# Kernel tuning notes

Hardware: AMD Instinct MI355X
Metric: run time of the kernel (lower is better)

## Reference

```python
import jax, jax.numpy as jnp
import numpy as np

EPS = 1e-7

def squash(s, axis=-1):
    # s * ||s||^2 / (1 + ||s||^2) / ||s||
    sq_norm = jnp.sum(jnp.square(s), axis=axis, keepdims=True)
    scale = sq_norm / (1.0 + sq_norm) / jnp.sqrt(sq_norm + EPS)
    return scale * s

def setup_inputs() -> dict:
    key = jax.random.key(0)
    k1, k2 = jax.random.split(key)
    B, I, K = 64, 2048, 16   # batch, input_num_capsule, input_dim_capsule
    N, D = 32, 32            # num_capsule, dim_capsule
    inputs = jax.random.normal(k1, (B, I, K), dtype=jnp.float32)
    W = jax.random.normal(k2, (N, I, D, K), dtype=jnp.float32) * 0.05
    return {"inputs": inputs, "W": W}

def reference(inputs, W, routings=3):
    # u_hat[b,n,i,d] = sum_k inputs[b,i,k] * W[n,i,d,k]
    # (tile over n + per-sample batch_dot in the original, fused here)
    u_hat = jnp.einsum('bik,nidk->bnid', inputs, W)  # [B,N,I,D]
    B, N, I, D = u_hat.shape
    b = jnp.zeros((B, N, I), dtype=u_hat.dtype)
    outputs = None
    for r in range(routings):
        c = jax.nn.softmax(b, axis=1)                          # softmax over num_capsule
        s = jnp.einsum('bni,bnid->bnd', c, u_hat)              # weighted sum over input caps
        outputs = squash(s)                                    # [B,N,D]
        if r < routings - 1:
            b = b + jnp.einsum('bnd,bnid->bni', outputs, u_hat)  # agreement update
    return outputs
```

## Files before the change

### kernel.cpp

```cpp
#include <hip/hip_runtime.h>
#include <hip/hip_bf16.h>
#include <math.h>

#define B_ 64
#define I_ 2048
#define K_ 16
#define N_ 32
#define D_ 32
#define SCH_ 16

typedef __attribute__((ext_vector_type(8))) short short8_t;
typedef __attribute__((ext_vector_type(4))) float f32x4_t;

#define OFF_INT   0u
#define OFF_CT    2097152u
#define OFF_BT    6291456u
#define OFF_SPART 10485760u
#define OFF_OFRAG 11534336u
#define OFF_XFRAG 11599872u
#define OFF_WFS   12648448u
#define OFF_WFU   29425664u

__device__ __forceinline__ unsigned int pk_bf16(float lo, float hi) {
    union { __hip_bfloat162 h2; unsigned int u; } cv;
    cv.h2 = __float22bfloat162_rn(float2{lo, hi});
    return cv.u;
}

__global__ __launch_bounds__(256) void k_prep(const float* __restrict__ in,
                                              float* __restrict__ inT,
                                              uint4* __restrict__ xfrag) {
    __shared__ float lds[B_][K_ + 1];
    const int i = blockIdx.x;
    const int t = threadIdx.x;
    const int b = t >> 2, kq = t & 3;
    const float4 v = *(const float4*)(in + ((size_t)b * I_ + i) * K_ + kq * 4);
    lds[b][kq * 4 + 0] = v.x; lds[b][kq * 4 + 1] = v.y;
    lds[b][kq * 4 + 2] = v.z; lds[b][kq * 4 + 3] = v.w;
    __syncthreads();
#pragma unroll
    for (int q = 0; q < 4; ++q) {
        const int j = t + q * 256;
        const int k = j >> 6, bb = j & 63;
        inT[(size_t)i * (K_ * B_) + j] = lds[bb][k];
    }
    if (t < 128) {
        const int m = t >> 5, r = t & 31, gl = r >> 4, kl = r & 15;
        const int bb = m * 16 + kl, k0 = 8 * gl;
        union { unsigned int u[4]; uint4 q; } o;
#pragma unroll
        for (int p = 0; p < 4; ++p)
            o.u[p] = pk_bf16(lds[bb][k0 + 2 * p], lds[bb][k0 + 2 * p + 1]);
        xfrag[((size_t)m * 1024 + (i >> 1)) * 64 + (2 * (i & 1) + gl) * 16 + kl] = o.q;
    }
}

__global__ __launch_bounds__(256) void k_wpack(const float* __restrict__ W,
                                               uint4* __restrict__ wfs,
                                               uint4* __restrict__ wfu) {
    __shared__ __align__(16) float lds[2048];
    const int c = blockIdx.x;
    const int n = blockIdx.y;
    const int t = threadIdx.x;
    const float4* s4 = (const float4*)(W + ((size_t)n * I_ + c * 4) * 512);
    float4* d4 = (float4*)lds;
    d4[t] = s4[t];
    d4[t + 256] = s4[t + 256];
    __syncthreads();
    {
        const int il = t >> 6, l = t & 63, g = l >> 4, kl = l & 15;
        const float* base = lds + il * 512;
        union { unsigned int u[4]; uint4 q; } o;
#pragma unroll
        for (int p = 0; p < 4; ++p)
            o.u[p] = pk_bf16(base[(8 * g + 2 * p) * 16 + kl],
                             base[(8 * g + 2 * p + 1) * 16 + kl]);
        wfu[((size_t)n * I_ + c * 4 + il) * 64 + l] = o.q;
    }
    {
        const int kkl = t >> 7, r = t & 127, nt = r >> 6, l = r & 63, g = l >> 4;
        const float* p = lds + kkl * 1024 + (g >> 1) * 512 + nt * 256
                         + (l & 15) * 16 + (g & 1) * 8;
        const float4 f0 = *(const float4*)p;
        const float4 f1 = *(const float4*)(p + 4);
        union { unsigned int u[4]; uint4 q; } o;
        o.u[0] = pk_bf16(f0.x, f0.y); o.u[1] = pk_bf16(f0.z, f0.w);
        o.u[2] = pk_bf16(f1.x, f1.y); o.u[3] = pk_bf16(f1.z, f1.w);
        wfs[(((size_t)n * 1024 + c * 2 + kkl) * 2 + nt) * 64 + l] = o.q;
    }
}

template<int UNIFORM>
__global__ __launch_bounds__(512, 2) void k_sweep_mfma(const uint4* __restrict__ wfs,
                                                       const uint4* __restrict__ xfrag,
                                                       const float* __restrict__ cT,
                                                       float* __restrict__ spart) {
    __shared__ float red[2][B_][D_ + 1];
    const int n = blockIdx.y, ch = blockIdx.x;
    const int t = threadIdx.x, w = t >> 6, l = t & 63;
    const int m = w >> 1, ks = w & 1;

    f32x4_t acc0 = {0.f, 0.f, 0.f, 0.f};
    f32x4_t acc1 = {0.f, 0.f, 0.f, 0.f};

    const uint4* xf = xfrag + (size_t)m * 65536 + l;
    const uint4* wf = wfs + (size_t)n * (1024 * 128) + l;
    const int kk0 = ch * 64 + ks * 32;

    for (int tt = 0; tt < 32; ++tt) {
        const int kk = kk0 + tt;
        union { uint4 q; unsigned int u[4]; } xv;
        xv.q = xf[(size_t)kk * 64];
        union { unsigned int u[4]; short8_t v; } af;
        if (UNIFORM) {
            af.u[0] = xv.u[0]; af.u[1] = xv.u[1];
            af.u[2] = xv.u[2]; af.u[3] = xv.u[3];
        } else {
            const float c = cT[((size_t)n * I_ + 2 * kk + (l >> 5)) * B_
                               + m * 16 + (l & 15)];
#pragma unroll
            for (int p = 0; p < 4; ++p) {
                const unsigned int uu = xv.u[p];
                const float lo = __uint_as_float(uu << 16);
                const float hi = __uint_as_float(uu & 0xffff0000u);
                af.u[p] = pk_bf16(lo * c, hi * c);
            }
        }
        union { uint4 q; short8_t v; } b0, b1;
        b0.q = wf[(size_t)kk * 128];
        b1.q = wf[(size_t)kk * 128 + 64];

        acc0 = __builtin_amdgcn_mfma_f32_16x16x32_bf16(af.v, b0.v, acc0, 0, 0, 0);
        acc1 = __builtin_amdgcn_mfma_f32_16x16x32_bf16(af.v, b1.v, acc1, 0, 0, 0);
    }

#pragma unroll
    for (int r = 0; r < 4; ++r) {
        const int row = m * 16 + (l >> 4) * 4 + r;
        red[ks][row][(l & 15)]      = acc0[r];
        red[ks][row][16 + (l & 15)] = acc1[r];
    }
    __syncthreads();
#pragma unroll
    for (int q = 0; q < 4; ++q) {
        const int j = q * 512 + t;
        const int b = j >> 5, d = j & 31;
        spart[((size_t)n * SCH_ + ch) * (B_ * D_) + j] = red[0][b][d] + red[1][b][d];
    }
}

template<int FINAL>
__global__ __launch_bounds__(256) void k_reduce(const float* __restrict__ spart,
                                                unsigned int* __restrict__ ofrag_u32,
                                                float* __restrict__ out,
                                                float prescale) {
    const int gt = blockIdx.x * 256 + threadIdx.x;
    const int n = gt >> 11;
    const int rem = gt & 2047;
    const int b = rem >> 5, d = rem & 31;
    const float* sp = spart + (size_t)n * (SCH_ * B_ * D_) + rem;
    float s = 0.f;
#pragma unroll
    for (int p = 0; p < SCH_; ++p) s += sp[p * (B_ * D_)];
    s *= prescale;

    float sq = s * s;
#pragma unroll
    for (int off = 16; off >= 1; off >>= 1) sq += __shfl_xor(sq, off, 64);
    const float scale = sq / ((1.0f + sq) * sqrtf(sq + 1e-7f));
    const float o = scale * s;
    if (FINAL) {
        out[((size_t)b * N_ + n) * D_ + d] = o;
    } else {
        const float o_next = __shfl_down(o, 1, 64);
        if ((d & 1) == 0) {
            const unsigned int val = pk_bf16(o, o_next);
            const int l = (d >> 3) * 16 + (b & 15);
            ofrag_u32[(((n * 4 + (b >> 4)) * 64) + l) * 4 + ((d & 7) >> 1)] = val;
        }
    }
}

template<int FIRST>
__global__ __launch_bounds__(512, 2) void k_updsm(const uint4* __restrict__ wfu,
                                                  const float* __restrict__ inT,
                                                  const uint4* __restrict__ ofrag,
                                                  float* __restrict__ bT,
                                                  float* __restrict__ cT) {
    const int t = threadIdx.x, w = t >> 6, l = t & 63;
    const int btile = w & 3;
    const int i = blockIdx.x * 2 + (w >> 2);
    const int g = l >> 4, kl = l & 15;
    const int bp = btile * 16 + kl;

    float x4[4];
    {
        const float* xp = inT + (size_t)i * (K_ * B_) + bp;
#pragma unroll
        for (int r = 0; r < 4; ++r) x4[r] = xp[(4 * g + r) * B_];
    }

    float bn[N_];
#pragma unroll
    for (int n = 0; n < N_; ++n) {
        union { uint4 q; short8_t v; } of, af;
        of.q = ofrag[(n * 4 + btile) * 64 + l];
        af.q = wfu[((size_t)n * I_ + i) * 64 + l];
        f32x4_t acc = {0.f, 0.f, 0.f, 0.f};
        acc = __builtin_amdgcn_mfma_f32_16x16x32_bf16(af.v, of.v, acc, 0, 0, 0);
        float gp = 0.f;
#pragma unroll
        for (int r = 0; r < 4; ++r) gp = fmaf(acc[r], x4[r], gp);
        gp += __shfl_xor(gp, 16, 64);
        gp += __shfl_xor(gp, 32, 64);
        const size_t bi = ((size_t)n * I_ + i) * B_ + bp;
        if (FIRST) {
            if (l < 16) bT[bi] = gp;
        } else {
            gp += bT[bi];
        }
        bn[n] = gp;
    }

    float mx = bn[0];
#pragma unroll
    for (int n = 1; n < N_; ++n) mx = fmaxf(mx, bn[n]);
    float sum = 0.f;
#pragma unroll
    for (int n = 0; n < N_; ++n) { bn[n] = __expf(bn[n] - mx); sum += bn[n]; }
    const float inv = 1.0f / sum;
    if (l < 16) {
#pragma unroll
        for (int n = 0; n < N_; ++n)
            cT[((size_t)n * I_ + i) * B_ + bp] = bn[n] * inv;
    }
}

extern "C" void kernel_launch(void* const* d_in, const int* in_sizes, int n_in,
                              void* d_out, int out_size, void* d_ws, size_t ws_size,
                              hipStream_t stream) {
    const float* inputs = (const float*)d_in[0];
    const float* W      = (const float*)d_in[1];
    float* out = (float*)d_out;
    float* ws  = (float*)d_ws;
    float* inT   = ws + OFF_INT;
    float* cT    = ws + OFF_CT;
    float* bT    = ws + OFF_BT;
    float* spart = ws + OFF_SPART;
    unsigned int* ofrag_u32 = (unsigned int*)(ws + OFF_OFRAG);
    uint4* ofrag = (uint4*)(ws + OFF_OFRAG);
    uint4* xfrag = (uint4*)(ws + OFF_XFRAG);
    uint4* wfs   = (uint4*)(ws + OFF_WFS);
    uint4* wfu   = (uint4*)(ws + OFF_WFU);

    k_prep<<<I_, 256, 0, stream>>>(inputs, inT, xfrag);
    k_wpack<<<dim3(512, N_), 256, 0, stream>>>(W, wfs, wfu);
    k_sweep_mfma<1><<<dim3(SCH_, N_), 512, 0, stream>>>(wfs, xfrag, cT, spart);
    k_reduce<0><<<256, 256, 0, stream>>>(spart, ofrag_u32, out, 1.0f / N_);
    k_updsm<1><<<I_ / 2, 512, 0, stream>>>(wfu, inT, ofrag, bT, cT);
    k_sweep_mfma<0><<<dim3(SCH_, N_), 512, 0, stream>>>(wfs, xfrag, cT, spart);
    k_reduce<0><<<256, 256, 0, stream>>>(spart, ofrag_u32, out, 1.0f);
    k_updsm<0><<<I_ / 2, 512, 0, stream>>>(wfu, inT, ofrag, bT, cT);
    k_sweep_mfma<0><<<dim3(SCH_, N_), 512, 0, stream>>>(wfs, xfrag, cT, spart);
    k_reduce<1><<<256, 256, 0, stream>>>(spart, ofrag_u32, out, 1.0f);
}
```

Before: 175.6 us.

## Use single plain bf16 copy of W for both sweep and agreement kernels

Replaces the two fragment-packed bf16 copies of W (wfs and wfu) with one straight bf16 conversion of W in its original layout, produced by a simple streaming kernel. Both the sweep and update kernels now index this shared buffer directly. The update kernel is restructured so each wave handles two input capsules: it computes x·W via MFMA with zero-masked halves, then dots the result with fp32 outputs read from a plain oT buffer, replacing the packed ofrag and the fp32 transposed inputs. The goal is to halve the weight packing writes and the workspace footprint, at the cost of doubled MFMA count and less fragment-friendly, more strided loads in the update kernel.

```diff
diff --git a/kernel.cpp b/kernel.cpp
--- a/kernel.cpp
+++ b/kernel.cpp
@@ -12,14 +12,12 @@
 typedef __attribute__((ext_vector_type(8))) short short8_t;
 typedef __attribute__((ext_vector_type(4))) float f32x4_t;
 
-#define OFF_INT   0u
-#define OFF_CT    2097152u
-#define OFF_BT    6291456u
-#define OFF_SPART 10485760u
-#define OFF_OFRAG 11534336u
-#define OFF_XFRAG 11599872u
-#define OFF_WFS   12648448u
-#define OFF_WFU   29425664u
+#define OFF_CT    0u
+#define OFF_BT    4194304u
+#define OFF_SPART 8388608u
+#define OFF_OT    9437184u
+#define OFF_XFRAG 9502720u
+#define OFF_WBF   10551296u
 
 __device__ __forceinline__ unsigned int pk_bf16(float lo, float hi) {
     union { __hip_bfloat162 h2; unsigned int u; } cv;
@@ -27,8 +25,19 @@
     return cv.u;
 }
 
+__global__ __launch_bounds__(256) void k_wconv(const float* __restrict__ W,
+                                               uint4* __restrict__ wbf4) {
+    const size_t tid = (size_t)blockIdx.x * 256 + threadIdx.x;
+    const float4* W4 = (const float4*)W;
+    const float4 a = W4[2 * tid];
+    const float4 b = W4[2 * tid + 1];
+    uint4 o;
+    o.x = pk_bf16(a.x, a.y); o.y = pk_bf16(a.z, a.w);
+    o.z = pk_bf16(b.x, b.y); o.w = pk_bf16(b.z, b.w);
+    wbf4[tid] = o;
+}
+
 __global__ __launch_bounds__(256) void k_prep(const float* __restrict__ in,
-                                              float* __restrict__ inT,
                                               uint4* __restrict__ xfrag) {
     __shared__ float lds[B_][K_ + 1];
     const int i = blockIdx.x;
@@ -38,12 +47,6 @@
     lds[b][kq * 4 + 0] = v.x; lds[b][kq * 4 + 1] = v.y;
     lds[b][kq * 4 + 2] = v.z; lds[b][kq * 4 + 3] = v.w;
     __syncthreads();
-#pragma unroll
-    for (int q = 0; q < 4; ++q) {
-        const int j = t + q * 256;
-        const int k = j >> 6, bb = j & 63;
-        inT[(size_t)i * (K_ * B_) + j] = lds[bb][k];
-    }
     if (t < 128) {
         const int m = t >> 5, r = t & 31, gl = r >> 4, kl = r & 15;
         const int bb = m * 16 + kl, k0 = 8 * gl;
@@ -55,43 +58,8 @@
     }
 }
 
-__global__ __launch_bounds__(256) void k_wpack(const float* __restrict__ W,
-                                               uint4* __restrict__ wfs,
-                                               uint4* __restrict__ wfu) {
-    __shared__ __align__(16) float lds[2048];
-    const int c = blockIdx.x;
-    const int n = blockIdx.y;
-    const int t = threadIdx.x;
-    const float4* s4 = (const float4*)(W + ((size_t)n * I_ + c * 4) * 512);
-    float4* d4 = (float4*)lds;
-    d4[t] = s4[t];
-    d4[t + 256] = s4[t + 256];
-    __syncthreads();
-    {
-        const int il = t >> 6, l = t & 63, g = l >> 4, kl = l & 15;
-        const float* base = lds + il * 512;
-        union { unsigned int u[4]; uint4 q; } o;
-#pragma unroll
-        for (int p = 0; p < 4; ++p)
-            o.u[p] = pk_bf16(base[(8 * g + 2 * p) * 16 + kl],
-                             base[(8 * g + 2 * p + 1) * 16 + kl]);
-        wfu[((size_t)n * I_ + c * 4 + il) * 64 + l] = o.q;
-    }
-    {
-        const int kkl = t >> 7, r = t & 127, nt = r >> 6, l = r & 63, g = l >> 4;
-        const float* p = lds + kkl * 1024 + (g >> 1) * 512 + nt * 256
-                         + (l & 15) * 16 + (g & 1) * 8;
-        const float4 f0 = *(const float4*)p;
-        const float4 f1 = *(const float4*)(p + 4);
-        union { unsigned int u[4]; uint4 q; } o;
-        o.u[0] = pk_bf16(f0.x, f0.y); o.u[1] = pk_bf16(f0.z, f0.w);
-        o.u[2] = pk_bf16(f1.x, f1.y); o.u[3] = pk_bf16(f1.z, f1.w);
-        wfs[(((size_t)n * 1024 + c * 2 + kkl) * 2 + nt) * 64 + l] = o.q;
-    }
-}
-
 template<int UNIFORM>
-__global__ __launch_bounds__(512, 2) void k_sweep_mfma(const uint4* __restrict__ wfs,
+__global__ __launch_bounds__(512, 2) void k_sweep_mfma(const uint4* __restrict__ wbf4,
                                                        const uint4* __restrict__ xfrag,
                                                        const float* __restrict__ cT,
                                                        float* __restrict__ spart) {
@@ -99,12 +67,14 @@
     const int n = blockIdx.y, ch = blockIdx.x;
     const int t = threadIdx.x, w = t >> 6, l = t & 63;
     const int m = w >> 1, ks = w & 1;
+    const int g = l >> 4;
 
     f32x4_t acc0 = {0.f, 0.f, 0.f, 0.f};
     f32x4_t acc1 = {0.f, 0.f, 0.f, 0.f};
 
     const uint4* xf = xfrag + (size_t)m * 65536 + l;
-    const uint4* wf = wfs + (size_t)n * (1024 * 128) + l;
+    const uint4* wb = wbf4 + (size_t)n * (I_ * 64)
+                    + (size_t)(g >> 1) * 64 + (l & 15) * 2 + (g & 1);
     const int kk0 = ch * 64 + ks * 32;
 
     for (int tt = 0; tt < 32; ++tt) {
@@ -127,8 +97,8 @@
             }
         }
         union { uint4 q; short8_t v; } b0, b1;
-        b0.q = wf[(size_t)kk * 128];
-        b1.q = wf[(size_t)kk * 128 + 64];
+        b0.q = wb[(size_t)kk * 128];
+        b1.q = wb[(size_t)kk * 128 + 32];
 
         acc0 = __builtin_amdgcn_mfma_f32_16x16x32_bf16(af.v, b0.v, acc0, 0, 0, 0);
         acc1 = __builtin_amdgcn_mfma_f32_16x16x32_bf16(af.v, b1.v, acc1, 0, 0, 0);
@@ -151,7 +121,7 @@
 
 template<int FINAL>
 __global__ __launch_bounds__(256) void k_reduce(const float* __restrict__ spart,
-                                                unsigned int* __restrict__ ofrag_u32,
+                                                float* __restrict__ oT,
                                                 float* __restrict__ out,
                                                 float prescale) {
     const int gt = blockIdx.x * 256 + threadIdx.x;
@@ -172,67 +142,79 @@
     if (FINAL) {
         out[((size_t)b * N_ + n) * D_ + d] = o;
     } else {
-        const float o_next = __shfl_down(o, 1, 64);
-        if ((d & 1) == 0) {
-            const unsigned int val = pk_bf16(o, o_next);
-            const int l = (d >> 3) * 16 + (b & 15);
-            ofrag_u32[(((n * 4 + (b >> 4)) * 64) + l) * 4 + ((d & 7) >> 1)] = val;
-        }
+        oT[gt] = o;
     }
 }
 
 template<int FIRST>
-__global__ __launch_bounds__(512, 2) void k_updsm(const uint4* __restrict__ wfu,
-                                                  const float* __restrict__ inT,
-                                                  const uint4* __restrict__ ofrag,
+__global__ __launch_bounds__(512, 2) void k_updsm(const uint4* __restrict__ wbf4,
+                                                  const uint4* __restrict__ xfrag,
+                                                  const float* __restrict__ oT,
                                                   float* __restrict__ bT,
                                                   float* __restrict__ cT) {
     const int t = threadIdx.x, w = t >> 6, l = t & 63;
     const int btile = w & 3;
-    const int i = blockIdx.x * 2 + (w >> 2);
+    const int p = blockIdx.x * 2 + (w >> 2);
+    const int i_e = 2 * p;
     const int g = l >> 4, kl = l & 15;
     const int bp = btile * 16 + kl;
 
-    float x4[4];
-    {
-        const float* xp = inT + (size_t)i * (K_ * B_) + bp;
-#pragma unroll
-        for (int r = 0; r < 4; ++r) x4[r] = xp[(4 * g + r) * B_];
-    }
-
-    float bn[N_];
+    union { uint4 q; short8_t v; } xf;
+    xf.q = xfrag[((size_t)btile * 1024 + p) * 64 + l];
+
+    const int i_l = i_e + (g >> 1);
+    const uint4* wrow = wbf4 + (size_t)i_l * 64 + kl * 2 + (g & 1);
+    const uint4 z4 = {0u, 0u, 0u, 0u};
+
+    float bne[N_], bno[N_];
 #pragma unroll
     for (int n = 0; n < N_; ++n) {
-        union { uint4 q; short8_t v; } of, af;
-        of.q = ofrag[(n * 4 + btile) * 64 + l];
-        af.q = wfu[((size_t)n * I_ + i) * 64 + l];
-        f32x4_t acc = {0.f, 0.f, 0.f, 0.f};
-        acc = __builtin_amdgcn_mfma_f32_16x16x32_bf16(af.v, of.v, acc, 0, 0, 0);
-        float gp = 0.f;
-#pragma unroll
-        for (int r = 0; r < 4; ++r) gp = fmaf(acc[r], x4[r], gp);
-        gp += __shfl_xor(gp, 16, 64);
-        gp += __shfl_xor(gp, 32, 64);
-        const size_t bi = ((size_t)n * I_ + i) * B_ + bp;
+        const uint4* wb = wrow + (size_t)n * (I_ * 64);
+        const float* op = oT + (size_t)n * 2048 + bp * 32 + 4 * g;
+        float ge = 0.f, go = 0.f;
+#pragma unroll
+        for (int h = 0; h < 2; ++h) {
+            union { uint4 q; short8_t v; } av, ae, ao;
+            av.q = wb[32 * h];
+            ae.q = (g < 2) ? av.q : z4;
+            ao.q = (g < 2) ? z4 : av.q;
+            f32x4_t ce = {0.f, 0.f, 0.f, 0.f};
+            f32x4_t co = {0.f, 0.f, 0.f, 0.f};
+            ce = __builtin_amdgcn_mfma_f32_16x16x32_bf16(ae.v, xf.v, ce, 0, 0, 0);
+            co = __builtin_amdgcn_mfma_f32_16x16x32_bf16(ao.v, xf.v, co, 0, 0, 0);
+            const float4 o4 = *(const float4*)(op + 16 * h);
+            ge += ce[0] * o4.x + ce[1] * o4.y + ce[2] * o4.z + ce[3] * o4.w;
+            go += co[0] * o4.x + co[1] * o4.y + co[2] * o4.z + co[3] * o4.w;
+        }
+        ge += __shfl_xor(ge, 16, 64);  ge += __shfl_xor(ge, 32, 64);
+        go += __shfl_xor(go, 16, 64);  go += __shfl_xor(go, 32, 64);
+        const size_t be = ((size_t)n * I_ + i_e) * B_ + bp;
         if (FIRST) {
-            if (l < 16) bT[bi] = gp;
+            if (l < 16) { bT[be] = ge; bT[be + B_] = go; }
         } else {
-            gp += bT[bi];
-        }
-        bn[n] = gp;
-    }
-
-    float mx = bn[0];
-#pragma unroll
-    for (int n = 1; n < N_; ++n) mx = fmaxf(mx, bn[n]);
-    float sum = 0.f;
-#pragma unroll
-    for (int n = 0; n < N_; ++n) { bn[n] = __expf(bn[n] - mx); sum += bn[n]; }
-    const float inv = 1.0f / sum;
+            ge += bT[be];
+            go += bT[be + B_];
+        }
+        bne[n] = ge;  bno[n] = go;
+    }
+
+    float me = bne[0], mo = bno[0];
+#pragma unroll
+    for (int n = 1; n < N_; ++n) { me = fmaxf(me, bne[n]); mo = fmaxf(mo, bno[n]); }
+    float se = 0.f, so = 0.f;
+#pragma unroll
+    for (int n = 0; n < N_; ++n) {
+        bne[n] = __expf(bne[n] - me); se += bne[n];
+        bno[n] = __expf(bno[n] - mo); so += bno[n];
+    }
+    const float ie = 1.0f / se, io = 1.0f / so;
     if (l < 16) {
 #pragma unroll
-        for (int n = 0; n < N_; ++n)
-            cT[((size_t)n * I_ + i) * B_ + bp] = bn[n] * inv;
+        for (int n = 0; n < N_; ++n) {
+            const size_t ce = ((size_t)n * I_ + i_e) * B_ + bp;
+            cT[ce]      = bne[n] * ie;
+            cT[ce + B_] = bno[n] * io;
+        }
     }
 }
 
@@ -243,24 +225,21 @@
     const float* W      = (const float*)d_in[1];
     float* out = (float*)d_out;
     float* ws  = (float*)d_ws;
-    float* inT   = ws + OFF_INT;
     float* cT    = ws + OFF_CT;
     float* bT    = ws + OFF_BT;
     float* spart = ws + OFF_SPART;
-    unsigned int* ofrag_u32 = (unsigned int*)(ws + OFF_OFRAG);
-    uint4* ofrag = (uint4*)(ws + OFF_OFRAG);
+    float* oT    = ws + OFF_OT;
     uint4* xfrag = (uint4*)(ws + OFF_XFRAG);
-    uint4* wfs   = (uint4*)(ws + OFF_WFS);
-    uint4* wfu   = (uint4*)(ws + OFF_WFU);
-
-    k_prep<<<I_, 256, 0, stream>>>(inputs, inT, xfrag);
-    k_wpack<<<dim3(512, N_), 256, 0, stream>>>(W, wfs, wfu);
-    k_sweep_mfma<1><<<dim3(SCH_, N_), 512, 0, stream>>>(wfs, xfrag, cT, spart);
-    k_reduce<0><<<256, 256, 0, stream>>>(spart, ofrag_u32, out, 1.0f / N_);
-    k_updsm<1><<<I_ / 2, 512, 0, stream>>>(wfu, inT, ofrag, bT, cT);
-    k_sweep_mfma<0><<<dim3(SCH_, N_), 512, 0, stream>>>(wfs, xfrag, cT, spart);
-    k_reduce<0><<<256, 256, 0, stream>>>(spart, ofrag_u32, out, 1.0f);
-    k_updsm<0><<<I_ / 2, 512, 0, stream>>>(wfu, inT, ofrag, bT, cT);
-    k_sweep_mfma<0><<<dim3(SCH_, N_), 512, 0, stream>>>(wfs, xfrag, cT, spart);
-    k_reduce<1><<<256, 256, 0, stream>>>(spart, ofrag_u32, out, 1.0f);
-}
+    uint4* wbf4  = (uint4*)(ws + OFF_WBF);
+
+    k_wconv<<<(N_ * I_ * D_ * K_) / (8 * 256), 256, 0, stream>>>(W, wbf4);
+    k_prep<<<I_, 256, 0, stream>>>(inputs, xfrag);
+    k_sweep_mfma<1><<<dim3(SCH_, N_), 512, 0, stream>>>(wbf4, xfrag, cT, spart);
+    k_reduce<0><<<256, 256, 0, stream>>>(spart, oT, out, 1.0f / N_);
+    k_updsm<1><<<I_ / 4, 512, 0, stream>>>(wbf4, xfrag, oT, bT, cT);
+    k_sweep_mfma<0><<<dim3(SCH_, N_), 512, 0, stream>>>(wbf4, xfrag, cT, spart);
+    k_reduce<0><<<256, 256, 0, stream>>>(spart, oT, out, 1.0f);
+    k_updsm<0><<<I_ / 4, 512, 0, stream>>>(wbf4, xfrag, oT, bT, cT);
+    k_sweep_mfma<0><<<dim3(SCH_, N_), 512, 0, stream>>>(wbf4, xfrag, cT, spart);
+    k_reduce<1><<<256, 256, 0, stream>>>(spart, oT, out, 1.0f);
+}
```

Result: slower. 193.0 us (+9.9%).

## Replace dual packed weight layouts with single plain bf16 conversion of W

Applied to the files above, without the earlier changes.

Drops the LDS-transposing k_wpack kernel that produced two separate MFMA-fragment copies of W, and instead converts W once to bf16 in its natural layout. The sweep kernel indexes the natural layout directly for its B fragments, and the update kernel assembles A fragments from 32-bit word loads with half-word shuffling. This halves the packed-weight write traffic and workspace but makes the update kernel's weight loads narrower and less contiguous.

```diff
diff --git a/kernel.cpp b/kernel.cpp
--- a/kernel.cpp
+++ b/kernel.cpp
@@ -18,13 +18,24 @@
 #define OFF_SPART 10485760u
 #define OFF_OFRAG 11534336u
 #define OFF_XFRAG 11599872u
-#define OFF_WFS   12648448u
-#define OFF_WFU   29425664u
+#define OFF_WBF   12648448u
 
 __device__ __forceinline__ unsigned int pk_bf16(float lo, float hi) {
     union { __hip_bfloat162 h2; unsigned int u; } cv;
     cv.h2 = __float22bfloat162_rn(float2{lo, hi});
     return cv.u;
+}
+
+__global__ __launch_bounds__(256) void k_wconv(const float* __restrict__ W,
+                                               uint4* __restrict__ wbf4) {
+    const size_t tid = (size_t)blockIdx.x * 256 + threadIdx.x;
+    const float4* W4 = (const float4*)W;
+    const float4 a = W4[2 * tid];
+    const float4 b = W4[2 * tid + 1];
+    uint4 o;
+    o.x = pk_bf16(a.x, a.y); o.y = pk_bf16(a.z, a.w);
+    o.z = pk_bf16(b.x, b.y); o.w = pk_bf16(b.z, b.w);
+    wbf4[tid] = o;
 }
 
 __global__ __launch_bounds__(256) void k_prep(const float* __restrict__ in,
@@ -55,43 +66,8 @@
     }
 }
 
-__global__ __launch_bounds__(256) void k_wpack(const float* __restrict__ W,
-                                               uint4* __restrict__ wfs,
-                                               uint4* __restrict__ wfu) {
-    __shared__ __align__(16) float lds[2048];
-    const int c = blockIdx.x;
-    const int n = blockIdx.y;
-    const int t = threadIdx.x;
-    const float4* s4 = (const float4*)(W + ((size_t)n * I_ + c * 4) * 512);
-    float4* d4 = (float4*)lds;
-    d4[t] = s4[t];
-    d4[t + 256] = s4[t + 256];
-    __syncthreads();
-    {
-        const int il = t >> 6, l = t & 63, g = l >> 4, kl = l & 15;
-        const float* base = lds + il * 512;
-        union { unsigned int u[4]; uint4 q; } o;
-#pragma unroll
-        for (int p = 0; p < 4; ++p)
-            o.u[p] = pk_bf16(base[(8 * g + 2 * p) * 16 + kl],
-                             base[(8 * g + 2 * p + 1) * 16 + kl]);
-        wfu[((size_t)n * I_ + c * 4 + il) * 64 + l] = o.q;
-    }
-    {
-        const int kkl = t >> 7, r = t & 127, nt = r >> 6, l = r & 63, g = l >> 4;
-        const float* p = lds + kkl * 1024 + (g >> 1) * 512 + nt * 256
-                         + (l & 15) * 16 + (g & 1) * 8;
-        const float4 f0 = *(const float4*)p;
-        const float4 f1 = *(const float4*)(p + 4);
-        union { unsigned int u[4]; uint4 q; } o;
-        o.u[0] = pk_bf16(f0.x, f0.y); o.u[1] = pk_bf16(f0.z, f0.w);
-        o.u[2] = pk_bf16(f1.x, f1.y); o.u[3] = pk_bf16(f1.z, f1.w);
-        wfs[(((size_t)n * 1024 + c * 2 + kkl) * 2 + nt) * 64 + l] = o.q;
-    }
-}
-
 template<int UNIFORM>
-__global__ __launch_bounds__(512, 2) void k_sweep_mfma(const uint4* __restrict__ wfs,
+__global__ __launch_bounds__(512, 2) void k_sweep_mfma(const uint4* __restrict__ wbf4,
                                                        const uint4* __restrict__ xfrag,
                                                        const float* __restrict__ cT,
                                                        float* __restrict__ spart) {
@@ -99,12 +75,14 @@
     const int n = blockIdx.y, ch = blockIdx.x;
     const int t = threadIdx.x, w = t >> 6, l = t & 63;
     const int m = w >> 1, ks = w & 1;
+    const int g = l >> 4;
 
     f32x4_t acc0 = {0.f, 0.f, 0.f, 0.f};
     f32x4_t acc1 = {0.f, 0.f, 0.f, 0.f};
 
     const uint4* xf = xfrag + (size_t)m * 65536 + l;
-    const uint4* wf = wfs + (size_t)n * (1024 * 128) + l;
+    const uint4* wb = wbf4 + (size_t)n * (I_ * 64)
+                    + (size_t)(g >> 1) * 64 + (l & 15) * 2 + (g & 1);
     const int kk0 = ch * 64 + ks * 32;
 
     for (int tt = 0; tt < 32; ++tt) {
@@ -127,8 +105,8 @@
             }
         }
         union { uint4 q; short8_t v; } b0, b1;
-        b0.q = wf[(size_t)kk * 128];
-        b1.q = wf[(size_t)kk * 128 + 64];
+        b0.q = wb[(size_t)kk * 128];
+        b1.q = wb[(size_t)kk * 128 + 32];
 
         acc0 = __builtin_amdgcn_mfma_f32_16x16x32_bf16(af.v, b0.v, acc0, 0, 0, 0);
         acc1 = __builtin_amdgcn_mfma_f32_16x16x32_bf16(af.v, b1.v, acc1, 0, 0, 0);
@@ -182,7 +160,7 @@
 }
 
 template<int FIRST>
-__global__ __launch_bounds__(512, 2) void k_updsm(const uint4* __restrict__ wfu,
+__global__ __launch_bounds__(512, 2) void k_updsm(const unsigned int* __restrict__ wbfu,
                                                   const float* __restrict__ inT,
                                                   const uint4* __restrict__ ofrag,
                                                   float* __restrict__ bT,
@@ -192,6 +170,8 @@
     const int i = blockIdx.x * 2 + (w >> 2);
     const int g = l >> 4, kl = l & 15;
     const int bp = btile * 16 + kl;
+    const int kh = kl >> 1;
+    const bool odd = (kl & 1) != 0;
 
     float x4[4];
     {
@@ -200,12 +180,23 @@
         for (int r = 0; r < 4; ++r) x4[r] = xp[(4 * g + r) * B_];
     }
 
+    const unsigned int* wr = wbfu + (size_t)i * 256 + 64 * g + kh;
+
     float bn[N_];
 #pragma unroll
     for (int n = 0; n < N_; ++n) {
         union { uint4 q; short8_t v; } of, af;
         of.q = ofrag[(n * 4 + btile) * 64 + l];
-        af.q = wfu[((size_t)n * I_ + i) * 64 + l];
+        const unsigned int* wn = wr + (size_t)n * (I_ * 256);
+        union { unsigned int u[4]; short8_t v; } au;
+#pragma unroll
+        for (int p = 0; p < 4; ++p) {
+            const unsigned int A = wn[16 * p];
+            const unsigned int Bv = wn[16 * p + 8];
+            au.u[p] = odd ? ((A >> 16) | (Bv & 0xffff0000u))
+                          : ((A & 0xffffu) | (Bv << 16));
+        }
+        af.q = *(uint4*)&au;
         f32x4_t acc = {0.f, 0.f, 0.f, 0.f};
         acc = __builtin_amdgcn_mfma_f32_16x16x32_bf16(af.v, of.v, acc, 0, 0, 0);
         float gp = 0.f;
@@ -250,17 +241,17 @@
     unsigned int* ofrag_u32 = (unsigned int*)(ws + OFF_OFRAG);
     uint4* ofrag = (uint4*)(ws + OFF_OFRAG);
     uint4* xfrag = (uint4*)(ws + OFF_XFRAG);
-    uint4* wfs   = (uint4*)(ws + OFF_WFS);
-    uint4* wfu   = (uint4*)(ws + OFF_WFU);
-
+    uint4* wbf4  = (uint4*)(ws + OFF_WBF);
+    const unsigned int* wbfu = (const unsigned int*)(ws + OFF_WBF);
+
+    k_wconv<<<(N_ * I_ * D_ * K_) / (8 * 256), 256, 0, stream>>>(W, wbf4);
     k_prep<<<I_, 256, 0, stream>>>(inputs, inT, xfrag);
-    k_wpack<<<dim3(512, N_), 256, 0, stream>>>(W, wfs, wfu);
-    k_sweep_mfma<1><<<dim3(SCH_, N_), 512, 0, stream>>>(wfs, xfrag, cT, spart);
+    k_sweep_mfma<1><<<dim3(SCH_, N_), 512, 0, stream>>>(wbf4, xfrag, cT, spart);
     k_reduce<0><<<256, 256, 0, stream>>>(spart, ofrag_u32, out, 1.0f / N_);
-    k_updsm<1><<<I_ / 2, 512, 0, stream>>>(wfu, inT, ofrag, bT, cT);
-    k_sweep_mfma<0><<<dim3(SCH_, N_), 512, 0, stream>>>(wfs, xfrag, cT, spart);
+    k_updsm<1><<<I_ / 2, 512, 0, stream>>>(wbfu, inT, ofrag, bT, cT);
+    k_sweep_mfma<0><<<dim3(SCH_, N_), 512, 0, stream>>>(wbf4, xfrag, cT, spart);
     k_reduce<0><<<256, 256, 0, stream>>>(spart, ofrag_u32, out, 1.0f);
-    k_updsm<0><<<I_ / 2, 512, 0, stream>>>(wfu, inT, ofrag, bT, cT);
-    k_sweep_mfma<0><<<dim3(SCH_, N_), 512, 0, stream>>>(wfs, xfrag, cT, spart);
+    k_updsm<0><<<I_ / 2, 512, 0, stream>>>(wbfu, inT, ofrag, bT, cT);
+    k_sweep_mfma<0><<<dim3(SCH_, N_), 512, 0, stream>>>(wbf4, xfrag, cT, spart);
     k_reduce<1><<<256, 256, 0, stream>>>(spart, ofrag_u32, out, 1.0f);
 }
```

Measured after the change: 225.9 us. 1.29x slower.
